# Performance work log

Hardware: AMD Instinct MI355X
Metric: run time of the kernel (lower is better)

## Reference

```python
import jax, jax.numpy as jnp
import numpy as np

NEG_SLOPE = 0.2  # PyG GATConv default negative_slope


def gat_conv(x, W, b, a_src, a_dst, src, dst, N, H, C):
    """PyG-style GATConv (v1 attention), concat heads, self-loops already in (src,dst)."""
    h = (x @ W).reshape(N, H, C)                       # [N,H,C]
    al_src = jnp.sum(h * a_src, axis=-1)               # [N,H]
    al_dst = jnp.sum(h * a_dst, axis=-1)               # [N,H]
    e = jax.nn.leaky_relu(al_src[src] + al_dst[dst], NEG_SLOPE)  # [E,H]
    m = jax.ops.segment_max(e, dst, num_segments=N)    # segment softmax (stable)
    m = jnp.where(jnp.isfinite(m), m, 0.0)
    ex = jnp.exp(e - m[dst])
    denom = jax.ops.segment_sum(ex, dst, num_segments=N)
    alpha = ex / (denom[dst] + 1e-16)                  # [E,H]
    msg = h[src] * alpha[..., None]                    # [E,H,C]
    out = jax.ops.segment_sum(msg, dst, num_segments=N)  # [N,H,C]
    return out.reshape(N, H * C) + b


def setup_inputs() -> dict:
    key = jax.random.key(0)
    ks = jax.random.split(key, 16)
    N, E, IN, HID, HEADS, OUT, G = 50000, 600000, 128, 64, 4, 10, 64
    x = jax.random.normal(ks[0], (N, IN), dtype=jnp.float32)
    edge_index = jax.random.randint(ks[1], (2, E), 0, N, dtype=jnp.int32)
    batch = jnp.sort(jax.random.randint(ks[2], (N,), 0, G, dtype=jnp.int32))
    s = 0.1
    p = {
        'W1': jax.random.normal(ks[3], (IN, HEADS * HID)) * s,
        'b1': jnp.zeros((HEADS * HID,), jnp.float32),
        'asrc1': jax.random.normal(ks[4], (HEADS, HID)) * s,
        'adst1': jax.random.normal(ks[5], (HEADS, HID)) * s,
        'W2': jax.random.normal(ks[6], (HEADS * HID, HEADS * HID)) * s,
        'b2': jnp.zeros((HEADS * HID,), jnp.float32),
        'asrc2': jax.random.normal(ks[7], (HEADS, HID)) * s,
        'adst2': jax.random.normal(ks[8], (HEADS, HID)) * s,
        'W3': jax.random.normal(ks[9], (HEADS * HID, HID)) * s,
        'b3': jnp.zeros((HID,), jnp.float32),
        'asrc3': jax.random.normal(ks[10], (1, HID)) * s,
        'adst3': jax.random.normal(ks[11], (1, HID)) * s,
        'linW': jax.random.normal(ks[12], (HID, OUT)) * s,
        'linb': jnp.zeros((OUT,), jnp.float32),
    }
    return dict(x=x, edge_index=edge_index, batch=batch, **p)


def reference(x, edge_index, batch, W1, b1, asrc1, adst1, W2, b2, asrc2, adst2,
              W3, b3, asrc3, adst3, linW, linb):
    N = x.shape[0]
    G = 64  # number of graphs
    loops = jnp.arange(N, dtype=edge_index.dtype)
    src = jnp.concatenate([edge_index[0], loops])  # PyG adds self-loops by default
    dst = jnp.concatenate([edge_index[1], loops])
    # eval mode: dropout is identity
    h = jax.nn.elu(gat_conv(x, W1, b1, asrc1, adst1, src, dst, N, 4, 64))
    h = jax.nn.elu(gat_conv(h, W2, b2, asrc2, adst2, src, dst, N, 4, 64))
    h = jax.nn.elu(gat_conv(h, W3, b3, asrc3, adst3, src, dst, N, 1, 64))
    # global mean pool over graphs
    sums = jax.ops.segment_sum(h, batch, num_segments=G)            # [G,64]
    cnts = jax.ops.segment_sum(jnp.ones((N,), h.dtype), batch, num_segments=G)
    pooled = sums / jnp.maximum(cnts, 1.0)[:, None]
    return pooled @ linW + linb                                      # [G,10]
```

## Files before the change

### kernel.cpp

```cpp
#include <hip/hip_runtime.h>
#include <hip/hip_bf16.h>
#include <math.h>

#define NEG_SLOPE 0.2f

typedef short short8 __attribute__((ext_vector_type(8)));
typedef float f32x4 __attribute__((ext_vector_type(4)));
typedef unsigned int u32;
typedef unsigned short u16;

__device__ __forceinline__ float lrelu(float x){ return x > 0.f ? x : NEG_SLOPE * x; }
__device__ __forceinline__ float elu_f(float x){ return x > 0.f ? x : __expf(x) - 1.f; }
__device__ __forceinline__ u16 f2bf(float f){
  __hip_bfloat16 h = __float2bfloat16(f);
  return *(u16*)&h;
}

__global__ void prep_kernel(const float* __restrict__ x, u16* __restrict__ xb, int n4,
                            const float* __restrict__ W1, u16* __restrict__ w1t,
                            const float* __restrict__ W2, u16* __restrict__ w2t,
                            const float* __restrict__ W3, u16* __restrict__ w3t,
                            int* __restrict__ cursor, int N,
                            float* __restrict__ sums, int* __restrict__ cnts){
  int i = blockIdx.x * 256 + threadIdx.x;
  if (i < n4){
    float4 v = ((const float4*)x)[i];
    ushort4 o;
    o.x = f2bf(v.x); o.y = f2bf(v.y); o.z = f2bf(v.z); o.w = f2bf(v.w);
    ((ushort4*)xb)[i] = o;
    return;
  }
  int t = i - n4;
  if (t < 128 * 256){
    int k = t >> 8, m = t & 255;
    w1t[m * 128 + k] = f2bf(W1[t]);
    return;
  }
  t -= 128 * 256;
  if (t < 256 * 256){
    int k = t >> 8, m = t & 255;
    w2t[m * 256 + k] = f2bf(W2[t]);
    return;
  }
  t -= 256 * 256;
  if (t < 256 * 64){
    int k = t >> 6, m = t & 63;
    w3t[m * 256 + k] = f2bf(W3[t]);
    return;
  }
  t -= 256 * 64;
  if (t < N){ cursor[t] = 0; return; }
  t -= N;
  if (t < 64 * 64){ sums[t] = 0.f; return; }
  t -= 64 * 64;
  if (t < 64) cnts[t] = 0;
}

__global__ void ell_kernel(const int* __restrict__ src, const int* __restrict__ dst,
                           int E, int N, int* cursor, int* __restrict__ ell){
  int i = blockIdx.x * 256 + threadIdx.x;
  if (i < E + N){
    int s, d;
    if (i < E){ s = src[i]; d = dst[i]; }
    else      { s = i - E;  d = i - E;  }
    int pos = atomicAdd(&cursor[d], 1);
    if (pos < 64) ell[(size_t)d * 64 + pos] = s;
  }
}

template<int BN>
__global__ __launch_bounds__(256) void gemm_mfma(const u16* __restrict__ A,
                                                 const u16* __restrict__ Bt,
                                                 u16* __restrict__ C,
                                                 const float* __restrict__ asrc,
                                                 const float* __restrict__ adst,
                                                 float* __restrict__ als,
                                                 float* __restrict__ ald,
                                                 int N, int K, int M){
  constexpr int BM = 128;
  constexpr int MI = (BN == 128) ? 4 : 2;
  constexpr int SB = BN * 8 / 256;
  constexpr int HH = (BN == 128) ? 4 : 1;
  __shared__ short As[8][BM][8];
  __shared__ short Bs[8][BN][8];
  const int tid = threadIdx.x;
  const int w = tid >> 6, lane = tid & 63;
  const int quad = lane >> 4, l16 = lane & 15;
  const int row0 = blockIdx.y * BM, col0 = blockIdx.x * BN;
  const int wrow = (BN == 128) ? (w >> 1) * 64 : w * 32;
  const int wcol = (BN == 128) ? (w & 1) * 64 : 0;

  f32x4 acc[MI][4];
#pragma unroll
  for (int i = 0; i < MI; i++)
#pragma unroll
    for (int j = 0; j < 4; j++) acc[i][j] = (f32x4){0.f, 0.f, 0.f, 0.f};

  for (int k0 = 0; k0 < K; k0 += 64){
    __syncthreads();
#pragma unroll
    for (int q = 0; q < 4; q++){
      int lb = q * 256 + w * 64;
      int li = lb + lane;
      int c = li >> 7, r = li & 127;
      int grow = min(row0 + r, N - 1);
      const u16* gp = A + (size_t)grow * K + k0 + c * 8;
      __builtin_amdgcn_global_load_lds((const __attribute__((address_space(1))) void*)gp,
                                       (__attribute__((address_space(3))) void*)((char*)&As[0][0][0] + (size_t)lb * 16),
                                       16, 0, 0);
    }
#pragma unroll
    for (int q = 0; q < SB; q++){
      int lb = q * 256 + w * 64;
      int li = lb + lane;
      int c = li / BN, n = li % BN;
      const u16* gp = Bt + (size_t)(col0 + n) * K + k0 + c * 8;
      __builtin_amdgcn_global_load_lds((const __attribute__((address_space(1))) void*)gp,
                                       (__attribute__((address_space(3))) void*)((char*)&Bs[0][0][0] + (size_t)lb * 16),
                                       16, 0, 0);
    }
    __syncthreads();
#pragma unroll
    for (int ks = 0; ks < 2; ks++){
      short8 a[MI], b[4];
#pragma unroll
      for (int i = 0; i < MI; i++) a[i] = *(const short8*)&As[ks * 4 + quad][wrow + i * 16 + l16][0];
#pragma unroll
      for (int j = 0; j < 4; j++)  b[j] = *(const short8*)&Bs[ks * 4 + quad][wcol + j * 16 + l16][0];
#pragma unroll
      for (int i = 0; i < MI; i++)
#pragma unroll
        for (int j = 0; j < 4; j++)
          acc[i][j] = __builtin_amdgcn_mfma_f32_16x16x32_bf16(a[i], b[j], acc[i][j], 0, 0, 0);
    }
  }

  const int head = (col0 + wcol) >> 6;
  float avs[4], avd[4];
#pragma unroll
  for (int j = 0; j < 4; j++){
    int c = j * 16 + l16;
    avs[j] = asrc[head * 64 + c];
    avd[j] = adst[head * 64 + c];
  }

#pragma unroll
  for (int i = 0; i < MI; i++){
#pragma unroll
    for (int rr = 0; rr < 4; rr++){
      int row = row0 + wrow + i * 16 + quad * 4 + rr;
      float ps = acc[i][0][rr] * avs[0] + acc[i][1][rr] * avs[1]
               + acc[i][2][rr] * avs[2] + acc[i][3][rr] * avs[3];
      float pd = acc[i][0][rr] * avd[0] + acc[i][1][rr] * avd[1]
               + acc[i][2][rr] * avd[2] + acc[i][3][rr] * avd[3];
#pragma unroll
      for (int off = 8; off > 0; off >>= 1){
        ps += __shfl_xor(ps, off);
        pd += __shfl_xor(pd, off);
      }
      if (row < N){
#pragma unroll
        for (int j = 0; j < 4; j++)
          C[(size_t)row * M + col0 + wcol + j * 16 + l16] = f2bf(acc[i][j][rr]);
        if (l16 == 0){
          als[(size_t)row * HH + head] = ps;
          ald[(size_t)row * HH + head] = pd;
        }
      }
    }
  }
}

template<bool OBF>
__global__ __launch_bounds__(256) void agg4_kernel(const u16* __restrict__ hb,
    const float* __restrict__ als, const float* __restrict__ ald,
    const int* __restrict__ degv, const int* __restrict__ ell,
    const float* __restrict__ bias, void* __restrict__ outv, int N){
  __shared__ float lex[4][256];
  __shared__ int lu[4][64];
  int wslot = threadIdx.x >> 6;
  int node = (blockIdx.x * 256 + threadIdx.x) >> 6;
  int lane = threadIdx.x & 63;
  if (node >= N) return;
  int deg = degv[node];
  float4 t4 = *(const float4*)(ald + node * 4);
  const int hh = lane >> 4;

  bool v = lane < deg;
  int u_raw = ell[(size_t)node * 64 + lane];
  int u = v ? u_raw : 0;
  float4 s = *(const float4*)(als + (size_t)u * 4);
  float4 exv;
  exv.x = v ? __expf(lrelu(s.x + t4.x)) : 0.f;
  exv.y = v ? __expf(lrelu(s.y + t4.y)) : 0.f;
  exv.z = v ? __expf(lrelu(s.z + t4.z)) : 0.f;
  exv.w = v ? __expf(lrelu(s.w + t4.w)) : 0.f;
  *(float4*)&lex[wslot][lane * 4] = exv;
  lu[wslot][lane] = u;
  asm volatile("s_waitcnt lgkmcnt(0)" ::: "memory");

  float a0 = 0.f, a1 = 0.f, a2 = 0.f, a3 = 0.f, denom = 0.f;
  const u16* hbl = hb + lane * 4;
#pragma unroll 8
  for (int jj = 0; jj < deg; jj++){
    float ex = lex[wslot][jj * 4 + hh];
    int uu = lu[wslot][jj];
    uint2 t = *(const uint2*)(hbl + (size_t)uu * 256);
    denom += ex;
    a0 += ex * __uint_as_float((t.x & 0xffffu) << 16);
    a1 += ex * __uint_as_float(t.x & 0xffff0000u);
    a2 += ex * __uint_as_float((t.y & 0xffffu) << 16);
    a3 += ex * __uint_as_float(t.y & 0xffff0000u);
  }
  float inv = 1.f / (denom + 1e-16f);
  int ch = lane * 4;
  float o0 = elu_f(a0 * inv + bias[ch]);
  float o1 = elu_f(a1 * inv + bias[ch + 1]);
  float o2 = elu_f(a2 * inv + bias[ch + 2]);
  float o3 = elu_f(a3 * inv + bias[ch + 3]);
  if (OBF){
    uint2 o;
    o.x = (u32)f2bf(o0) | ((u32)f2bf(o1) << 16);
    o.y = (u32)f2bf(o2) | ((u32)f2bf(o3) << 16);
    ((uint2*)outv)[(size_t)node * 64 + lane] = o;
  } else {
    *(float4*)((float*)outv + (size_t)node * 256 + ch) = make_float4(o0, o1, o2, o3);
  }
}

__global__ __launch_bounds__(256) void agg1_kernel(const u16* __restrict__ hb,
    const float* __restrict__ als, const float* __restrict__ ald,
    const int* __restrict__ degv, const int* __restrict__ ell,
    const float* __restrict__ bias, float* __restrict__ out, int N){
  __shared__ float lex[4][72];
  __shared__ int lu[4][72];
  int wslot = threadIdx.x >> 6;
  int node = (blockIdx.x * 256 + threadIdx.x) >> 6;
  int lane = threadIdx.x & 63;
  if (node >= N) return;
  int deg = degv[node];
  float adv = ald[node];

  bool v = lane < deg;
  int u_raw = ell[(size_t)node * 64 + lane];
  int u = v ? u_raw : 0;
  lex[wslot][lane] = v ? __expf(lrelu(als[u] + adv)) : 0.f;
  lu[wslot][lane] = u;
  if (lane < 8){ lex[wslot][64 + lane] = 0.f; lu[wslot][64 + lane] = 0; }
  asm volatile("s_waitcnt lgkmcnt(0)" ::: "memory");

  int eo = lane >> 4;
  int chb = (lane & 15) * 4;
  float a0 = 0.f, a1 = 0.f, a2 = 0.f, a3 = 0.f, denom = 0.f;
#pragma unroll 4
  for (int j2 = 0; j2 < deg; j2 += 4){
    int jj = j2 + eo;
    float ex = lex[wslot][jj];
    int uu = lu[wslot][jj];
    uint2 t = *(const uint2*)(hb + (size_t)uu * 64 + chb);
    denom += ex;
    a0 += ex * __uint_as_float((t.x & 0xffffu) << 16);
    a1 += ex * __uint_as_float(t.x & 0xffff0000u);
    a2 += ex * __uint_as_float((t.y & 0xffffu) << 16);
    a3 += ex * __uint_as_float(t.y & 0xffff0000u);
  }
#pragma unroll
  for (int off = 16; off < 64; off <<= 1){
    denom += __shfl_xor(denom, off);
    a0 += __shfl_xor(a0, off); a1 += __shfl_xor(a1, off);
    a2 += __shfl_xor(a2, off); a3 += __shfl_xor(a3, off);
  }
  if (eo == 0){
    float inv = 1.f / (denom + 1e-16f);
    float o0 = elu_f(a0 * inv + bias[chb]);
    float o1 = elu_f(a1 * inv + bias[chb + 1]);
    float o2 = elu_f(a2 * inv + bias[chb + 2]);
    float o3 = elu_f(a3 * inv + bias[chb + 3]);
    *(float4*)(out + (size_t)node * 64 + chb) = make_float4(o0, o1, o2, o3);
  }
}

__global__ void pool_kernel(const float* __restrict__ f, const int* __restrict__ batch,
                            float* sums, int* cnts, int N){
  int lane = threadIdx.x;
  int s = blockIdx.x * 128;
  if (s >= N) return;
  int e = min(s + 128, N);
  float acc = 0.f;
  int cnt = 0;
  int cur = batch[s];
  for (int n = s; n < e; n++){
    int g = batch[n];
    if (g != cur){
      atomicAdd(&sums[cur * 64 + lane], acc);
      if (lane == 0) atomicAdd(&cnts[cur], cnt);
      acc = 0.f; cnt = 0; cur = g;
    }
    acc += f[(size_t)n * 64 + lane];
    cnt++;
  }
  atomicAdd(&sums[cur * 64 + lane], acc);
  if (lane == 0) atomicAdd(&cnts[cur], cnt);
}

__global__ void final_kernel(const float* __restrict__ sums, const int* __restrict__ cnts,
                             const float* __restrict__ linW, const float* __restrict__ linb,
                             float* __restrict__ out){
  int t = threadIdx.x;
  if (t >= 640) return;
  int g = t / 10, o = t % 10;
  float c = fmaxf((float)cnts[g], 1.f);
  float acc = 0.f;
#pragma unroll
  for (int k = 0; k < 64; k++) acc += sums[g * 64 + k] * linW[k * 10 + o];
  out[t] = acc / c + linb[o];
}

extern "C" void kernel_launch(void* const* d_in, const int* in_sizes, int n_in,
                              void* d_out, int out_size, void* d_ws, size_t ws_size,
                              hipStream_t stream) {
  const float* x     = (const float*)d_in[0];
  const int*   ei    = (const int*)  d_in[1];
  const int*   batch = (const int*)  d_in[2];
  const float* W1    = (const float*)d_in[3];
  const float* b1    = (const float*)d_in[4];
  const float* asrc1 = (const float*)d_in[5];
  const float* adst1 = (const float*)d_in[6];
  const float* W2    = (const float*)d_in[7];
  const float* b2    = (const float*)d_in[8];
  const float* asrc2 = (const float*)d_in[9];
  const float* adst2 = (const float*)d_in[10];
  const float* W3    = (const float*)d_in[11];
  const float* b3    = (const float*)d_in[12];
  const float* asrc3 = (const float*)d_in[13];
  const float* adst3 = (const float*)d_in[14];
  const float* linW  = (const float*)d_in[15];
  const float* linb  = (const float*)d_in[16];

  const int N = in_sizes[0] / 128;
  const int E = in_sizes[1] / 2;
  const int Etot = E + N;
  const int G = 64;
  const int* src = ei;
  const int* dst = ei + E;

  char* p = (char*)d_ws;
  auto carve = [&](size_t bytes) -> char* {
    char* r = p;
    p += (bytes + 255) & ~(size_t)255;
    return r;
  };
  u16*   xb       = (u16*)  carve((size_t)N * 128 * 2);
  u16*   w1t      = (u16*)  carve((size_t)256 * 128 * 2);
  u16*   w2t      = (u16*)  carve((size_t)256 * 256 * 2);
  u16*   w3t      = (u16*)  carve((size_t)64 * 256 * 2);
  u16*   hb       = (u16*)  carve((size_t)N * 256 * 2);
  u16*   featb    = (u16*)  carve((size_t)N * 256 * 2);
  float* out3     = (float*)carve((size_t)N * 64 * 4);
  float* als      = (float*)carve((size_t)N * 4 * 4);
  float* ald      = (float*)carve((size_t)N * 4 * 4);
  int*   cursor   = (int*)  carve((size_t)N * 4);
  int*   ell      = (int*)  carve((size_t)N * 64 * 4);
  float* sums     = (float*)carve((size_t)G * 64 * 4);
  int*   cnts     = (int*)  carve((size_t)G * 4);

  const int n4 = N * 128 / 4;
  const int prep_items = n4 + 128 * 256 + 256 * 256 + 256 * 64 + N + G * 64 + G;

  prep_kernel<<<(prep_items + 255) / 256, 256, 0, stream>>>(x, xb, n4, W1, w1t, W2, w2t, W3, w3t,
                                                            cursor, N, sums, cnts);

  ell_kernel<<<(Etot + 255) / 256, 256, 0, stream>>>(src, dst, E, N, cursor, ell);

  const int nby = (N + 127) / 128;
  const int wpn_grid = (N + 3) / 4;

  gemm_mfma<128><<<dim3(2, nby), 256, 0, stream>>>(xb, w1t, hb, asrc1, adst1, als, ald, N, 128, 256);
  agg4_kernel<true><<<wpn_grid, 256, 0, stream>>>(hb, als, ald, cursor, ell, b1, featb, N);

  gemm_mfma<128><<<dim3(2, nby), 256, 0, stream>>>(featb, w2t, hb, asrc2, adst2, als, ald, N, 256, 256);
  agg4_kernel<true><<<wpn_grid, 256, 0, stream>>>(hb, als, ald, cursor, ell, b2, featb, N);

  gemm_mfma<64><<<dim3(1, nby), 256, 0, stream>>>(featb, w3t, hb, asrc3, adst3, als, ald, N, 256, 64);
  agg1_kernel<<<wpn_grid, 256, 0, stream>>>(hb, als, ald, cursor, ell, b3, out3, N);

  pool_kernel<<<(N + 127) / 128, 64, 0, stream>>>(out3, batch, sums, cnts, N);
  final_kernel<<<1, 640, 0, stream>>>(sums, cnts, linW, linb, (float*)d_out);
}
```

Before: 365.6 us.

## Use full-width 256-column GEMM tiles and handle self-loops implicitly in aggregation

The 256-output GEMMs now use one 512-thread block per row tile covering all columns, so the A tile is loaded once instead of twice. Self-loops are no longer inserted into the ELL lists through atomics; each aggregation kernel adds the node's own contribution directly. This removes N atomic inserts and the duplicate A traffic. The cost is larger blocks that may lower occupancy, and neighbour degree is now clamped to 64 explicitly.

```diff
diff --git a/kernel.cpp b/kernel.cpp
--- a/kernel.cpp
+++ b/kernel.cpp
@@ -11,6 +11,8 @@
 
 __device__ __forceinline__ float lrelu(float x){ return x > 0.f ? x : NEG_SLOPE * x; }
 __device__ __forceinline__ float elu_f(float x){ return x > 0.f ? x : __expf(x) - 1.f; }
+__device__ __forceinline__ float blo(u32 w){ return __uint_as_float(w << 16); }
+__device__ __forceinline__ float bhi(u32 w){ return __uint_as_float(w & 0xffff0000u); }
 __device__ __forceinline__ u16 f2bf(float f){
   __hip_bfloat16 h = __float2bfloat16(f);
   return *(u16*)&h;
@@ -57,38 +59,34 @@
 }
 
 __global__ void ell_kernel(const int* __restrict__ src, const int* __restrict__ dst,
-                           int E, int N, int* cursor, int* __restrict__ ell){
+                           int E, int* cursor, int* __restrict__ ell){
   int i = blockIdx.x * 256 + threadIdx.x;
-  if (i < E + N){
-    int s, d;
-    if (i < E){ s = src[i]; d = dst[i]; }
-    else      { s = i - E;  d = i - E;  }
+  if (i < E){
+    int s = src[i], d = dst[i];
     int pos = atomicAdd(&cursor[d], 1);
     if (pos < 64) ell[(size_t)d * 64 + pos] = s;
   }
 }
 
 template<int BN>
-__global__ __launch_bounds__(256) void gemm_mfma(const u16* __restrict__ A,
-                                                 const u16* __restrict__ Bt,
-                                                 u16* __restrict__ C,
-                                                 const float* __restrict__ asrc,
-                                                 const float* __restrict__ adst,
-                                                 float* __restrict__ als,
-                                                 float* __restrict__ ald,
-                                                 int N, int K, int M){
-  constexpr int BM = 128;
-  constexpr int MI = (BN == 128) ? 4 : 2;
-  constexpr int SB = BN * 8 / 256;
-  constexpr int HH = (BN == 128) ? 4 : 1;
-  __shared__ short As[8][BM][8];
+__global__ __launch_bounds__((BN == 256) ? 512 : 256) void gemm_mfma(
+    const u16* __restrict__ A, const u16* __restrict__ Bt, u16* __restrict__ C,
+    const float* __restrict__ asrc, const float* __restrict__ adst,
+    float* __restrict__ als, float* __restrict__ ald, int N, int K, int M){
+  constexpr int T  = (BN == 256) ? 512 : 256;
+  constexpr int MI = (BN == 256) ? 4 : 2;
+  constexpr int HH = BN / 64;
+  constexpr int AQ = 1024 / T;
+  constexpr int SB = BN * 8 / T;
+  constexpr int LB = (BN == 256) ? 8 : 6;
+  __shared__ short As[8][128][8];
   __shared__ short Bs[8][BN][8];
   const int tid = threadIdx.x;
   const int w = tid >> 6, lane = tid & 63;
   const int quad = lane >> 4, l16 = lane & 15;
-  const int row0 = blockIdx.y * BM, col0 = blockIdx.x * BN;
-  const int wrow = (BN == 128) ? (w >> 1) * 64 : w * 32;
-  const int wcol = (BN == 128) ? (w & 1) * 64 : 0;
+  const int row0 = blockIdx.y * 128;
+  const int wrow = (BN == 256) ? (w >> 2) * 64 : w * 32;
+  const int wcol = (BN == 256) ? (w & 3) * 64 : 0;
 
   f32x4 acc[MI][4];
 #pragma unroll
@@ -99,8 +97,8 @@
   for (int k0 = 0; k0 < K; k0 += 64){
     __syncthreads();
 #pragma unroll
-    for (int q = 0; q < 4; q++){
-      int lb = q * 256 + w * 64;
+    for (int q = 0; q < AQ; q++){
+      int lb = q * T + w * 64;
       int li = lb + lane;
       int c = li >> 7, r = li & 127;
       int grow = min(row0 + r, N - 1);
@@ -111,10 +109,10 @@
     }
 #pragma unroll
     for (int q = 0; q < SB; q++){
-      int lb = q * 256 + w * 64;
+      int lb = q * T + w * 64;
       int li = lb + lane;
-      int c = li / BN, n = li % BN;
-      const u16* gp = Bt + (size_t)(col0 + n) * K + k0 + c * 8;
+      int c = li >> LB, n = li & (BN - 1);
+      const u16* gp = Bt + (size_t)n * K + k0 + c * 8;
       __builtin_amdgcn_global_load_lds((const __attribute__((address_space(1))) void*)gp,
                                        (__attribute__((address_space(3))) void*)((char*)&Bs[0][0][0] + (size_t)lb * 16),
                                        16, 0, 0);
@@ -135,7 +133,7 @@
     }
   }
 
-  const int head = (col0 + wcol) >> 6;
+  const int head = wcol >> 6;
   float avs[4], avd[4];
 #pragma unroll
   for (int j = 0; j < 4; j++){
@@ -161,7 +159,7 @@
       if (row < N){
 #pragma unroll
         for (int j = 0; j < 4; j++)
-          C[(size_t)row * M + col0 + wcol + j * 16 + l16] = f2bf(acc[i][j][rr]);
+          C[(size_t)row * M + wcol + j * 16 + l16] = f2bf(acc[i][j][rr]);
         if (l16 == 0){
           als[(size_t)row * HH + head] = ps;
           ald[(size_t)row * HH + head] = pd;
@@ -171,24 +169,22 @@
   }
 }
 
-template<bool OBF>
 __global__ __launch_bounds__(256) void agg4_kernel(const u16* __restrict__ hb,
     const float* __restrict__ als, const float* __restrict__ ald,
     const int* __restrict__ degv, const int* __restrict__ ell,
-    const float* __restrict__ bias, void* __restrict__ outv, int N){
+    const float* __restrict__ bias, u16* __restrict__ out, int N){
   __shared__ float lex[4][256];
   __shared__ int lu[4][64];
   int wslot = threadIdx.x >> 6;
   int node = (blockIdx.x * 256 + threadIdx.x) >> 6;
   int lane = threadIdx.x & 63;
   if (node >= N) return;
-  int deg = degv[node];
+  int deg = min(degv[node], 64);
   float4 t4 = *(const float4*)(ald + node * 4);
   const int hh = lane >> 4;
 
   bool v = lane < deg;
-  int u_raw = ell[(size_t)node * 64 + lane];
-  int u = v ? u_raw : 0;
+  int u = v ? ell[(size_t)node * 64 + lane] : 0;
   float4 s = *(const float4*)(als + (size_t)u * 4);
   float4 exv;
   exv.x = v ? __expf(lrelu(s.x + t4.x)) : 0.f;
@@ -199,18 +195,28 @@
   lu[wslot][lane] = u;
   asm volatile("s_waitcnt lgkmcnt(0)" ::: "memory");
 
-  float a0 = 0.f, a1 = 0.f, a2 = 0.f, a3 = 0.f, denom = 0.f;
   const u16* hbl = hb + lane * 4;
+  float4 ss = *(const float4*)(als + (size_t)node * 4);
+  float es0 = __expf(lrelu(ss.x + t4.x));
+  float es1 = __expf(lrelu(ss.y + t4.y));
+  float es2 = __expf(lrelu(ss.z + t4.z));
+  float es3 = __expf(lrelu(ss.w + t4.w));
+  float exs = (hh == 0) ? es0 : (hh == 1) ? es1 : (hh == 2) ? es2 : es3;
+  uint2 tself = *(const uint2*)(hbl + (size_t)node * 256);
+  float denom = exs;
+  float a0 = exs * blo(tself.x), a1 = exs * bhi(tself.x);
+  float a2 = exs * blo(tself.y), a3 = exs * bhi(tself.y);
+
 #pragma unroll 8
   for (int jj = 0; jj < deg; jj++){
     float ex = lex[wslot][jj * 4 + hh];
     int uu = lu[wslot][jj];
     uint2 t = *(const uint2*)(hbl + (size_t)uu * 256);
     denom += ex;
-    a0 += ex * __uint_as_float((t.x & 0xffffu) << 16);
-    a1 += ex * __uint_as_float(t.x & 0xffff0000u);
-    a2 += ex * __uint_as_float((t.y & 0xffffu) << 16);
-    a3 += ex * __uint_as_float(t.y & 0xffff0000u);
+    a0 += ex * blo(t.x);
+    a1 += ex * bhi(t.x);
+    a2 += ex * blo(t.y);
+    a3 += ex * bhi(t.y);
   }
   float inv = 1.f / (denom + 1e-16f);
   int ch = lane * 4;
@@ -218,14 +224,10 @@
   float o1 = elu_f(a1 * inv + bias[ch + 1]);
   float o2 = elu_f(a2 * inv + bias[ch + 2]);
   float o3 = elu_f(a3 * inv + bias[ch + 3]);
-  if (OBF){
-    uint2 o;
-    o.x = (u32)f2bf(o0) | ((u32)f2bf(o1) << 16);
-    o.y = (u32)f2bf(o2) | ((u32)f2bf(o3) << 16);
-    ((uint2*)outv)[(size_t)node * 64 + lane] = o;
-  } else {
-    *(float4*)((float*)outv + (size_t)node * 256 + ch) = make_float4(o0, o1, o2, o3);
-  }
+  uint2 o;
+  o.x = (u32)f2bf(o0) | ((u32)f2bf(o1) << 16);
+  o.y = (u32)f2bf(o2) | ((u32)f2bf(o3) << 16);
+  ((uint2*)out)[(size_t)node * 64 + lane] = o;
 }
 
 __global__ __launch_bounds__(256) void agg1_kernel(const u16* __restrict__ hb,
@@ -238,12 +240,11 @@
   int node = (blockIdx.x * 256 + threadIdx.x) >> 6;
   int lane = threadIdx.x & 63;
   if (node >= N) return;
-  int deg = degv[node];
+  int deg = min(degv[node], 64);
   float adv = ald[node];
 
   bool v = lane < deg;
-  int u_raw = ell[(size_t)node * 64 + lane];
-  int u = v ? u_raw : 0;
+  int u = v ? ell[(size_t)node * 64 + lane] : 0;
   lex[wslot][lane] = v ? __expf(lrelu(als[u] + adv)) : 0.f;
   lu[wslot][lane] = u;
   if (lane < 8){ lex[wslot][64 + lane] = 0.f; lu[wslot][64 + lane] = 0; }
@@ -252,6 +253,13 @@
   int eo = lane >> 4;
   int chb = (lane & 15) * 4;
   float a0 = 0.f, a1 = 0.f, a2 = 0.f, a3 = 0.f, denom = 0.f;
+  if (eo == 0){
+    float exs = __expf(lrelu(als[node] + adv));
+    uint2 t = *(const uint2*)(hb + (size_t)node * 64 + chb);
+    denom = exs;
+    a0 = exs * blo(t.x); a1 = exs * bhi(t.x);
+    a2 = exs * blo(t.y); a3 = exs * bhi(t.y);
+  }
 #pragma unroll 4
   for (int j2 = 0; j2 < deg; j2 += 4){
     int jj = j2 + eo;
@@ -259,10 +267,10 @@
     int uu = lu[wslot][jj];
     uint2 t = *(const uint2*)(hb + (size_t)uu * 64 + chb);
     denom += ex;
-    a0 += ex * __uint_as_float((t.x & 0xffffu) << 16);
-    a1 += ex * __uint_as_float(t.x & 0xffff0000u);
-    a2 += ex * __uint_as_float((t.y & 0xffffu) << 16);
-    a3 += ex * __uint_as_float(t.y & 0xffff0000u);
+    a0 += ex * blo(t.x);
+    a1 += ex * bhi(t.x);
+    a2 += ex * blo(t.y);
+    a3 += ex * bhi(t.y);
   }
 #pragma unroll
   for (int off = 16; off < 64; off <<= 1){
@@ -339,7 +347,6 @@
 
   const int N = in_sizes[0] / 128;
   const int E = in_sizes[1] / 2;
-  const int Etot = E + N;
   const int G = 64;
   const int* src = ei;
   const int* dst = ei + E;
@@ -370,16 +377,16 @@
   prep_kernel<<<(prep_items + 255) / 256, 256, 0, stream>>>(x, xb, n4, W1, w1t, W2, w2t, W3, w3t,
                                                             cursor, N, sums, cnts);
 
-  ell_kernel<<<(Etot + 255) / 256, 256, 0, stream>>>(src, dst, E, N, cursor, ell);
+  ell_kernel<<<(E + 255) / 256, 256, 0, stream>>>(src, dst, E, cursor, ell);
 
   const int nby = (N + 127) / 128;
   const int wpn_grid = (N + 3) / 4;
 
-  gemm_mfma<128><<<dim3(2, nby), 256, 0, stream>>>(xb, w1t, hb, asrc1, adst1, als, ald, N, 128, 256);
-  agg4_kernel<true><<<wpn_grid, 256, 0, stream>>>(hb, als, ald, cursor, ell, b1, featb, N);
-
-  gemm_mfma<128><<<dim3(2, nby), 256, 0, stream>>>(featb, w2t, hb, asrc2, adst2, als, ald, N, 256, 256);
-  agg4_kernel<true><<<wpn_grid, 256, 0, stream>>>(hb, als, ald, cursor, ell, b2, featb, N);
+  gemm_mfma<256><<<dim3(1, nby), 512, 0, stream>>>(xb, w1t, hb, asrc1, adst1, als, ald, N, 128, 256);
+  agg4_kernel<<<wpn_grid, 256, 0, stream>>>(hb, als, ald, cursor, ell, b1, featb, N);
+
+  gemm_mfma<256><<<dim3(1, nby), 512, 0, stream>>>(featb, w2t, hb, asrc2, adst2, als, ald, N, 256, 256);
+  agg4_kernel<<<wpn_grid, 256, 0, stream>>>(hb, als, ald, cursor, ell, b2, featb, N);
 
   gemm_mfma<64><<<dim3(1, nby), 256, 0, stream>>>(featb, w3t, hb, asrc3, adst3, als, ald, N, 256, 64);
   agg1_kernel<<<wpn_grid, 256, 0, stream>>>(hb, als, ald, cursor, ell, b3, out3, N);
```

Result: no change. 366.3 us (+0.2%).
